# Optimization experiments

Hardware: AMD Instinct MI355X
Metric: run time of the kernel (lower is better)

The kernel has to match this reference:

```python
import jax, jax.numpy as jnp
import numpy as np

EPS = 1e-10

def conv1x1(x, W, b):
    # x:[B,C,H,W], W:[O,C], b:[O]
    return jnp.einsum('bchw,oc->bohw', x, W) + b[None, :, None, None]

def setup_inputs() -> dict:
    key = jax.random.key(0)
    ks = jax.random.split(key, 16)
    B, C, H, W = 8, 512, 32, 32
    R, heads = 4, 8
    s = 1.0 / np.sqrt(C)
    inp = {
        'x': jax.random.normal(ks[0], (B, C, H, W), jnp.float32),
        'u_q': jax.random.uniform(ks[1], (B, R, H, W), jnp.float32, minval=EPS, maxval=1.0),
        'u_k': jax.random.uniform(ks[2], (B, R, H, W), jnp.float32, minval=EPS, maxval=1.0),
        'wq_s': jax.random.normal(ks[3], (R, C), jnp.float32) * s,
        'bq_s': jnp.zeros((R,), jnp.float32),
        'wk_s': jax.random.normal(ks[4], (R, C), jnp.float32) * s,
        'bk_s': jnp.zeros((R,), jnp.float32),
        'Wq': jax.random.normal(ks[5], (C, C), jnp.float32) * s,
        'bq': jnp.zeros((C,), jnp.float32),
        'Wk': jax.random.normal(ks[6], (C, C), jnp.float32) * s,
        'bk': jnp.zeros((C,), jnp.float32),
        'Wv': jax.random.normal(ks[7], (C, C), jnp.float32) * s,
        'bv': jnp.zeros((C,), jnp.float32),
        'Wp': jax.random.normal(ks[8], (C, C), jnp.float32) * s,
        'bp': jnp.zeros((C,), jnp.float32),
    }
    return inp

def reference(x, u_q, u_k, wq_s, bq_s, wk_s, bk_s, Wq, bq, Wk, bk, Wv, bv, Wp, bp):
    B, C, H, W = x.shape
    heads = 8
    hd = C // heads
    scale = hd ** -0.5
    N = H * W

    # gumbel-softmax hard=True then take channel 0 == (argmax(logits+g, dim=1) == 0)
    def sel_mask(ws, bs, u):
        logits = conv1x1(x, ws, bs)                       # [B,R,H,W]
        g = -jnp.log(-jnp.log(u + EPS) + EPS)             # gumbel noise
        m = jnp.argmax(logits + g, axis=1) == 0           # [B,H,W] bool
        return m.reshape(B, N)

    mq = jax.lax.stop_gradient(sel_mask(wq_s, bq_s, u_q))  # selected query points
    mk = jax.lax.stop_gradient(sel_mask(wk_s, bk_s, u_k))  # selected key/value points

    q = conv1x1(x, Wq, bq).reshape(B, heads, hd, N)
    k = conv1x1(x, Wk, bk).reshape(B, heads, hd, N)
    v = conv1x1(x, Wv, bv).reshape(B, heads, hd, N)

    # attention restricted to selected key positions (softmax over masked set
    # == softmax over the gathered subset in the torch code)
    attn = jnp.einsum('bhdn,bhdm->bhnm', q * scale, k)     # [B,h,N,N]
    attn = jnp.where(mk[:, None, None, :], attn, -1e30)
    attn = jax.nn.softmax(attn, axis=-1)
    out = jnp.einsum('bhnm,bhdm->bhdn', attn, v)           # [B,h,hd,N]

    # scatter attention output back into v at the selected query positions
    v_new = jnp.where(mq[:, None, :], out.reshape(B, C, N), v.reshape(B, C, N))
    v_new = v_new.reshape(B, C, H, W)
    return conv1x1(v_new, Wp, bp)
```

## Files before the change

kernel.cpp:

```cpp
#include <hip/hip_runtime.h>
#include <hip/hip_bf16.h>

#define B_ 8
#define C_ 512
#define N_ 1024
#define HEADS_ 8
#define HD_ 64

using f32x4  = __attribute__((ext_vector_type(4))) float;
using bf16x8 = __attribute__((ext_vector_type(8))) __bf16;

__device__ __forceinline__ unsigned short f2bf(float f) {
  union { float f; unsigned u; } v; v.f = f;
  unsigned r = v.u + 0x7FFFu + ((v.u >> 16) & 1u);
  return (unsigned short)(r >> 16);
}

__device__ __forceinline__ void gload16(const void* g, void* l) {
  __builtin_amdgcn_global_load_lds(
      (const __attribute__((address_space(1))) unsigned int*)g,
      (__attribute__((address_space(3))) unsigned int*)l, 16, 0, 0);
}

__global__ __launch_bounds__(256) void k_prep(
    const float* __restrict__ x, const float* __restrict__ u_q, const float* __restrict__ u_k,
    const float* __restrict__ wqs, const float* __restrict__ bqs,
    const float* __restrict__ wks, const float* __restrict__ bks,
    const float* __restrict__ Wq, const float* __restrict__ Wk,
    const float* __restrict__ Wv, const float* __restrict__ Wp,
    unsigned short* __restrict__ xT, unsigned short* __restrict__ wbf,
    unsigned int* __restrict__ sel) {
  __shared__ __align__(16) char smem[25600];
  int id = blockIdx.x;
  int t = threadIdx.x;
  if (id < 256) {
    float* wq_l = (float*)smem;
    float* wk_l = wq_l + 2048;
    float* part = wk_l + 2048;
    int b = id >> 5;
    int n0 = (id & 31) * 32;
    int nl = t & 31, ch = t >> 5;
    for (int i = t; i < 2048; i += 256) {
      wq_l[i] = wqs[i];
      wk_l[i] = wks[i];
    }
    __syncthreads();
    int cbase = ch * 64;
    const float* xp = x + ((size_t)b * C_ + cbase) * N_ + n0 + nl;
    float sq[4] = {0.f, 0.f, 0.f, 0.f};
    float sk[4] = {0.f, 0.f, 0.f, 0.f};
    for (int c = 0; c < 64; c++) {
      float xv = xp[(size_t)c * N_];
#pragma unroll
      for (int r = 0; r < 4; r++) {
        sq[r] = fmaf(wq_l[r * 512 + cbase + c], xv, sq[r]);
        sk[r] = fmaf(wk_l[r * 512 + cbase + c], xv, sk[r]);
      }
    }
    float* pp = part + (ch * 32 + nl) * 9;
#pragma unroll
    for (int r = 0; r < 4; r++) { pp[r] = sq[r]; pp[4 + r] = sk[r]; }
    __syncthreads();
    if (t < 32) {
      int n = n0 + t;
      float fq[4], fk[4];
#pragma unroll
      for (int r = 0; r < 4; r++) { fq[r] = bqs[r]; fk[r] = bks[r]; }
#pragma unroll
      for (int c2 = 0; c2 < 8; c2++) {
        const float* q2 = part + (c2 * 32 + t) * 9;
#pragma unroll
        for (int r = 0; r < 4; r++) { fq[r] += q2[r]; fk[r] += q2[4 + r]; }
      }
#pragma unroll
      for (int r = 0; r < 4; r++) {
        float uq = u_q[((size_t)b * 4 + r) * N_ + n];
        float uk = u_k[((size_t)b * 4 + r) * N_ + n];
        fq[r] += -logf(-logf(uq + 1e-10f) + 1e-10f);
        fk[r] += -logf(-logf(uk + 1e-10f) + 1e-10f);
      }
      bool selq = (fq[0] >= fq[1]) && (fq[0] >= fq[2]) && (fq[0] >= fq[3]);
      bool selk = (fk[0] >= fk[1]) && (fk[0] >= fk[2]) && (fk[0] >= fk[3]);
      sel[(size_t)b * N_ + n] = selq ? 1u : 0u;
      sel[(size_t)(B_ + b) * N_ + n] = selk ? 1u : 0u;
    }
  } else if (id < 1280) {
    float (*tile)[65] = (float(*)[65])smem;
    int m = id - 256;
    int n0 = (m & 15) * 64, c0 = ((m >> 4) & 7) * 64, b = m >> 7;
    int tr = t >> 2, tc = (t & 3) * 16;
    const float* src = x + ((size_t)b * C_ + c0) * N_ + n0;
#pragma unroll
    for (int i = 0; i < 4; i++) {
      float4 v4 = *(const float4*)(src + (size_t)tr * N_ + tc + i * 4);
      tile[tr][tc + i * 4 + 0] = v4.x; tile[tr][tc + i * 4 + 1] = v4.y;
      tile[tr][tc + i * 4 + 2] = v4.z; tile[tr][tc + i * 4 + 3] = v4.w;
    }
    __syncthreads();
    unsigned short* dst = xT + ((size_t)b * N_ + n0) * C_ + c0;
#pragma unroll
    for (int i = 0; i < 4; i++) {
      unsigned short o4[4];
#pragma unroll
      for (int j = 0; j < 4; j++) o4[j] = f2bf(tile[tc + i * 4 + j][tr]);
      unsigned lo = (unsigned)o4[0] | ((unsigned)o4[1] << 16);
      unsigned hi = (unsigned)o4[2] | ((unsigned)o4[3] << 16);
      uint2 u; u.x = lo; u.y = hi;
      *(uint2*)(dst + (size_t)tr * C_ + tc + i * 4) = u;
    }
  } else {
    int i = (id - 1280) * 256 + t;
    int mat = i >> 16, idx4 = i & 65535;
    const float* src = (mat == 0) ? Wq : (mat == 1) ? Wk : (mat == 2) ? Wv : Wp;
    float4 v = ((const float4*)src)[idx4];
    unsigned lo = (unsigned)f2bf(v.x) | ((unsigned)f2bf(v.y) << 16);
    unsigned hi = (unsigned)f2bf(v.z) | ((unsigned)f2bf(v.w) << 16);
    uint2 u; u.x = lo; u.y = hi;
    ((uint2*)wbf)[i] = u;
  }
}

__global__ __launch_bounds__(1024) void k_scan(
    const unsigned int* __restrict__ sel, unsigned int* __restrict__ idx,
    unsigned int* __restrict__ cnt) {
  int which = blockIdx.x, b = blockIdx.y;
  const unsigned int* s = sel + ((size_t)which * B_ + b) * N_;
  unsigned int* ip = idx + ((size_t)which * B_ + b) * N_;
  int t = threadIdx.x, lane = t & 63, w = t >> 6;
  __shared__ unsigned int wtot[16], woff[16], totsh;
  unsigned int f = s[t];
  unsigned long long bal = __ballot(f != 0);
  unsigned int wpre = __popcll(bal & ((1ull << lane) - 1ull));
  if (lane == 0) wtot[w] = (unsigned int)__popcll(bal);
  __syncthreads();
  if (t == 0) {
    unsigned int acc = 0;
#pragma unroll
    for (int i = 0; i < 16; i++) { woff[i] = acc; acc += wtot[i]; }
    totsh = acc;
    cnt[which * B_ + b] = acc;
  }
  __syncthreads();
  unsigned int tot = totsh;
  if (f) ip[woff[w] + wpre] = (unsigned int)t;
  if (t >= (int)tot) ip[t] = 0u;
}

template <int MODE>
__global__ __launch_bounds__(256) void k_gemm(
    const unsigned short* __restrict__ Wall, const unsigned short* __restrict__ Bt,
    const float* __restrict__ bias0, const float* __restrict__ bias1,
    const float* __restrict__ bias2,
    const unsigned int* __restrict__ idx, const unsigned int* __restrict__ cnt,
    void* __restrict__ outv) {
  __shared__ __align__(16) unsigned short a_lds[2][128 * 64];
  __shared__ __align__(16) unsigned short b_lds[2][64 * 64];
  int z = blockIdx.z;
  int mat = (MODE == 0) ? (z >> 3) : 0;
  int b   = (MODE == 0) ? (z & 7) : z;
  int n0 = blockIdx.x * 64;
  if (MODE == 0 && mat < 2 && n0 >= (int)cnt[mat * B_ + b]) return;
  const unsigned short* A = Wall + (size_t)mat * 262144;
  const float* bias = (mat == 0) ? bias0 : (mat == 1) ? bias1 : bias2;
  int m0 = blockIdx.y * 128;
  int t = threadIdx.x, wave = t >> 6, lane = t & 63;
  int wr = (wave >> 1) * 64, wc = (wave & 1) * 32;
  f32x4 acc[4][2] = {};
  int srow = t >> 3, spch = t & 7;
  int lch = spch ^ (srow & 7);
  const unsigned short* aptr[4];
  const unsigned short* bptr[2];
#pragma unroll
  for (int i = 0; i < 4; i++)
    aptr[i] = A + (size_t)(m0 + srow + i * 32) * C_ + lch * 8;
#pragma unroll
  for (int i = 0; i < 2; i++) {
    int grow = n0 + srow + i * 32;
    int srcr = (MODE == 0 && mat < 2) ? (int)idx[((size_t)mat * B_ + b) * N_ + grow] : grow;
    bptr[i] = Bt + ((size_t)b * N_ + srcr) * C_ + lch * 8;
  }
#define STAGE_(buf, kt) do { int k0_ = (kt) * 64;                                          \
    _Pragma("unroll") for (int i_ = 0; i_ < 4; i_++)                                       \
      gload16(aptr[i_] + k0_, (char*)a_lds + (buf) * 16384 + wave * 1024 + i_ * 4096);     \
    _Pragma("unroll") for (int i_ = 0; i_ < 2; i_++)                                       \
      gload16(bptr[i_] + k0_, (char*)b_lds + (buf) * 8192 + wave * 1024 + i_ * 4096);      \
    } while (0)
  STAGE_(0, 0);
  for (int kt = 0; kt < 8; kt++) {
    int cur = kt & 1;
    if (kt < 7) {
      STAGE_(cur ^ 1, kt + 1);
      asm volatile("s_waitcnt vmcnt(6)" ::: "memory");
    } else {
      asm volatile("s_waitcnt vmcnt(0)" ::: "memory");
    }
    __builtin_amdgcn_s_barrier();
    const unsigned short* al = a_lds[cur];
    const unsigned short* bl = b_lds[cur];
#pragma unroll
    for (int ks = 0; ks < 2; ks++) {
      bf16x8 af[4], bfr[2];
#pragma unroll
      for (int mi = 0; mi < 4; mi++) {
        int row = wr + mi * 16 + (lane & 15);
        int pch = (ks * 4 + (lane >> 4)) ^ (row & 7);
        af[mi] = *(const bf16x8*)(al + row * 64 + pch * 8);
      }
#pragma unroll
      for (int ni = 0; ni < 2; ni++) {
        int row = wc + ni * 16 + (lane & 15);
        int pch = (ks * 4 + (lane >> 4)) ^ (row & 7);
        bfr[ni] = *(const bf16x8*)(bl + row * 64 + pch * 8);
      }
#pragma unroll
      for (int mi = 0; mi < 4; mi++)
#pragma unroll
        for (int ni = 0; ni < 2; ni++)
          acc[mi][ni] = __builtin_amdgcn_mfma_f32_16x16x32_bf16(af[mi], bfr[ni], acc[mi][ni], 0, 0, 0);
    }
    __builtin_amdgcn_s_barrier();
  }
#undef STAGE_
  if (MODE == 0) {
    unsigned short* outp = (unsigned short*)outv + (size_t)mat * B_ * N_ * C_ + (size_t)b * N_ * C_;
#pragma unroll
    for (int mi = 0; mi < 4; mi++) {
      int ob = m0 + wr + mi * 16 + ((lane >> 4) << 2);
      float bs[4];
#pragma unroll
      for (int r = 0; r < 4; r++) bs[r] = bias[ob + r];
#pragma unroll
      for (int ni = 0; ni < 2; ni++) {
        int n = n0 + wc + ni * 16 + (lane & 15);
        unsigned short o4[4];
#pragma unroll
        for (int r = 0; r < 4; r++) o4[r] = f2bf(acc[mi][ni][r] + bs[r]);
        unsigned lo = (unsigned)o4[0] | ((unsigned)o4[1] << 16);
        unsigned hi = (unsigned)o4[2] | ((unsigned)o4[3] << 16);
        uint2 u; u.x = lo; u.y = hi;
        *(uint2*)(outp + (size_t)n * C_ + ob) = u;
      }
    }
  } else {
    float* outp = (float*)outv + (size_t)b * C_ * N_;
#pragma unroll
    for (int mi = 0; mi < 4; mi++) {
      int ob = m0 + wr + mi * 16 + ((lane >> 4) << 2);
#pragma unroll
      for (int r = 0; r < 4; r++) {
        float bv = bias[ob + r];
#pragma unroll
        for (int ni = 0; ni < 2; ni++) {
          int n = n0 + wc + ni * 16 + (lane & 15);
          outp[(size_t)(ob + r) * N_ + n] = acc[mi][ni][r] + bv;
        }
      }
    }
  }
}

__global__ __launch_bounds__(256) void k_gather_vt(
    const unsigned short* __restrict__ vT, const unsigned int* __restrict__ idx,
    const unsigned int* __restrict__ cnt, unsigned short* __restrict__ vctr) {
  int b = blockIdx.z;
  unsigned int nk = cnt[B_ + b];
  int j0 = blockIdx.x * 64;
  if (j0 >= (int)nk) return;
  int c0 = blockIdx.y * 64;
  __shared__ unsigned short tile[64][72];
  int t = threadIdx.x, tr = t >> 2, tc = (t & 3) * 16;
  int jj = j0 + tr;
  bool valid = jj < (int)nk;
  unsigned int srow = valid ? idx[((size_t)B_ + b) * N_ + jj] : 0u;
  const unsigned short* src = vT + ((size_t)b * N_ + srow) * C_ + c0;
#pragma unroll
  for (int i = 0; i < 4; i++) {
    ushort4 v4 = {0, 0, 0, 0};
    if (valid) v4 = *(const ushort4*)(src + tc + i * 4);
    tile[tr][tc + i * 4 + 0] = v4.x; tile[tr][tc + i * 4 + 1] = v4.y;
    tile[tr][tc + i * 4 + 2] = v4.z; tile[tr][tc + i * 4 + 3] = v4.w;
  }
  __syncthreads();
  unsigned short* dst = vctr + ((size_t)b * C_ + c0) * N_ + j0;
#pragma unroll
  for (int i = 0; i < 4; i++) {
    unsigned short o4[4];
#pragma unroll
    for (int j = 0; j < 4; j++) o4[j] = tile[tc + i * 4 + j][tr];
    unsigned lo = (unsigned)o4[0] | ((unsigned)o4[1] << 16);
    unsigned hi = (unsigned)o4[2] | ((unsigned)o4[3] << 16);
    uint2 u; u.x = lo; u.y = hi;
    *(uint2*)(dst + (size_t)tr * N_ + tc + i * 4) = u;
  }
}

__global__ __launch_bounds__(256) void k_attn(
    const unsigned short* __restrict__ qc, const unsigned short* __restrict__ kc,
    const unsigned short* __restrict__ vctr, unsigned short* __restrict__ vnew,
    const unsigned int* __restrict__ idx, const unsigned int* __restrict__ cnt) {
  __shared__ __align__(16) unsigned short p_lds[4][16 * 72];
  __shared__ float macc[4][16][65];
  __shared__ float mml[4][2][16];
  int qt = blockIdx.x, h = blockIdx.y, b = blockIdx.z;
  int nq = (int)cnt[b], nk = (int)cnt[B_ + b];
  int q0 = qt * 16;
  if (q0 >= nq) return;
  int t = threadIdx.x, wave = t >> 6, lane = t & 63;
  const unsigned short* qp =
      qc + ((size_t)b * N_ + q0 + (lane & 15)) * C_ + h * HD_ + ((lane >> 4) * 8);
  bf16x8 qf0 = *(const bf16x8*)qp;
  bf16x8 qf1 = *(const bf16x8*)(qp + 32);
  float mrow[4], lrow[4];
  f32x4 acc[4];
#pragma unroll
  for (int r = 0; r < 4; r++) { mrow[r] = -1e30f; lrow[r] = 0.f; }
#pragma unroll
  for (int d = 0; d < 4; d++) acc[d] = f32x4{0.f, 0.f, 0.f, 0.f};
  for (int j0 = wave * 64; j0 < nk; j0 += 256) {
    f32x4 s[4];
#pragma unroll
    for (int nf = 0; nf < 4; nf++) {
      const unsigned short* kp =
          kc + ((size_t)b * N_ + j0 + nf * 16 + (lane & 15)) * C_ + h * HD_ + ((lane >> 4) * 8);
      bf16x8 kf0 = *(const bf16x8*)kp;
      bf16x8 kf1 = *(const bf16x8*)(kp + 32);
      f32x4 z = {0.f, 0.f, 0.f, 0.f};
      z = __builtin_amdgcn_mfma_f32_16x16x32_bf16(qf0, kf0, z, 0, 0, 0);
      z = __builtin_amdgcn_mfma_f32_16x16x32_bf16(qf1, kf1, z, 0, 0, 0);
      float mv = ((j0 + nf * 16 + (lane & 15)) < nk) ? 0.f : -1e30f;
#pragma unroll
      for (int r = 0; r < 4; r++) s[nf][r] = z[r] * 0.125f + mv;
    }
    float alpha[4];
#pragma unroll
    for (int r = 0; r < 4; r++) {
      float mx = fmaxf(fmaxf(s[0][r], s[1][r]), fmaxf(s[2][r], s[3][r]));
      mx = fmaxf(mx, __shfl_xor(mx, 1));
      mx = fmaxf(mx, __shfl_xor(mx, 2));
      mx = fmaxf(mx, __shfl_xor(mx, 4));
      mx = fmaxf(mx, __shfl_xor(mx, 8));
      float mn = fmaxf(mrow[r], mx);
      alpha[r] = __expf(mrow[r] - mn);
      mrow[r] = mn;
      float rs = 0.f;
      int ql = ((lane >> 4) << 2) + r;
#pragma unroll
      for (int nf = 0; nf < 4; nf++) {
        float sv = s[nf][r];
        float p = (sv < -1e29f) ? 0.f : __expf(sv - mn);
        rs += p;
        p_lds[wave][ql * 72 + nf * 16 + (lane & 15)] = f2bf(p);
      }
      rs += __shfl_xor(rs, 1);
      rs += __shfl_xor(rs, 2);
      rs += __shfl_xor(rs, 4);
      rs += __shfl_xor(rs, 8);
      lrow[r] = lrow[r] * alpha[r] + rs;
    }
    bf16x8 pa0 = *(const bf16x8*)&p_lds[wave][(lane & 15) * 72 + ((lane >> 4) * 8)];
    bf16x8 pa1 = *(const bf16x8*)&p_lds[wave][(lane & 15) * 72 + 32 + ((lane >> 4) * 8)];
#pragma unroll
    for (int df = 0; df < 4; df++) {
#pragma unroll
      for (int r = 0; r < 4; r++) acc[df][r] *= alpha[r];
      const unsigned short* vp =
          vctr + ((size_t)b * C_ + h * HD_ + df * 16 + (lane & 15)) * N_ + j0 + ((lane >> 4) * 8);
      bf16x8 vf0 = *(const bf16x8*)vp;
      bf16x8 vf1 = *(const bf16x8*)(vp + 32);
      acc[df] = __builtin_amdgcn_mfma_f32_16x16x32_bf16(pa0, vf0, acc[df], 0, 0, 0);
      acc[df] = __builtin_amdgcn_mfma_f32_16x16x32_bf16(pa1, vf1, acc[df], 0, 0, 0);
    }
  }
#pragma unroll
  for (int df = 0; df < 4; df++)
#pragma unroll
    for (int r = 0; r < 4; r++)
      macc[wave][((lane >> 4) << 2) + r][df * 16 + (lane & 15)] = acc[df][r];
  if ((lane & 15) == 0) {
#pragma unroll
    for (int r = 0; r < 4; r++) {
      mml[wave][0][((lane >> 4) << 2) + r] = mrow[r];
      mml[wave][1][((lane >> 4) << 2) + r] = lrow[r];
    }
  }
  __syncthreads();
  {
    int q = t >> 4, d0 = (t & 15) * 4;
    float mg = fmaxf(fmaxf(mml[0][0][q], mml[1][0][q]), fmaxf(mml[2][0][q], mml[3][0][q]));
    float lg = 0.f, o0 = 0.f, o1 = 0.f, o2 = 0.f, o3 = 0.f;
#pragma unroll
    for (int w = 0; w < 4; w++) {
      float sc = __expf(mml[w][0][q] - mg);
      lg += mml[w][1][q] * sc;
      o0 += macc[w][q][d0 + 0] * sc;
      o1 += macc[w][q][d0 + 1] * sc;
      o2 += macc[w][q][d0 + 2] * sc;
      o3 += macc[w][q][d0 + 3] * sc;
    }
    if (q0 + q < nq) {
      unsigned int qrow = idx[(size_t)b * N_ + q0 + q];
      float inv = 1.0f / lg;
      unsigned short o4[4] = {f2bf(o0 * inv), f2bf(o1 * inv), f2bf(o2 * inv), f2bf(o3 * inv)};
      unsigned lo = (unsigned)o4[0] | ((unsigned)o4[1] << 16);
      unsigned hi = (unsigned)o4[2] | ((unsigned)o4[3] << 16);
      uint2 u; u.x = lo; u.y = hi;
      *(uint2*)(vnew + ((size_t)b * N_ + qrow) * C_ + h * HD_ + d0) = u;
    }
  }
}

extern "C" void kernel_launch(void* const* d_in, const int* in_sizes, int n_in,
                              void* d_out, int out_size, void* d_ws, size_t ws_size,
                              hipStream_t stream) {
  const float* x   = (const float*)d_in[0];
  const float* u_q = (const float*)d_in[1];
  const float* u_k = (const float*)d_in[2];
  const float* wqs = (const float*)d_in[3];
  const float* bqs = (const float*)d_in[4];
  const float* wks = (const float*)d_in[5];
  const float* bks = (const float*)d_in[6];
  const float* Wq  = (const float*)d_in[7];
  const float* bq  = (const float*)d_in[8];
  const float* Wk  = (const float*)d_in[9];
  const float* bk  = (const float*)d_in[10];
  const float* Wv  = (const float*)d_in[11];
  const float* bv  = (const float*)d_in[12];
  const float* Wp  = (const float*)d_in[13];
  const float* bp  = (const float*)d_in[14];

  char* ws = (char*)d_ws;
  unsigned short* xT   = (unsigned short*)(ws);
  unsigned short* wbf  = (unsigned short*)(ws + 8388608);
  unsigned short* qkv  = (unsigned short*)(ws + 10485760);
  unsigned short* qc   = qkv;
  unsigned short* kc   = qkv + (size_t)B_ * N_ * C_;
  unsigned short* vT   = kc + (size_t)B_ * N_ * C_;
  unsigned short* vctr = (unsigned short*)(ws + 35651584);
  unsigned int*   sel  = (unsigned int*)(ws + 44040192);
  unsigned int*   idx  = (unsigned int*)(ws + 44105728);
  unsigned int*   cnt  = (unsigned int*)(ws + 44171264);

  k_prep<<<dim3(2304), 256, 0, stream>>>(x, u_q, u_k, wqs, bqs, wks, bks,
                                         Wq, Wk, Wv, Wp, xT, wbf, sel);
  k_scan<<<dim3(2, 8), 1024, 0, stream>>>(sel, idx, cnt);
  k_gemm<0><<<dim3(16, 4, 24), 256, 0, stream>>>(wbf, xT, bq, bk, bv, idx, cnt, (void*)qkv);
  k_gather_vt<<<dim3(16, 8, 8), 256, 0, stream>>>(vT, idx, cnt, vctr);
  k_attn<<<dim3(64, 8, 8), 256, 0, stream>>>(qc, kc, vctr, vT, idx, cnt);
  k_gemm<1><<<dim3(16, 4, 8), 256, 0, stream>>>(wbf + 3 * 262144, vT, bp, bp, bp, idx, cnt, d_out);
}
```

Baseline: 164.5 us.

## Fuse V gather-transpose into QKV GEMM epilogue and shrink GEMM M-tile

```diff
diff --git a/kernel.cpp b/kernel.cpp
--- a/kernel.cpp
+++ b/kernel.cpp
@@ -122,10 +122,11 @@
 
 __global__ __launch_bounds__(1024) void k_scan(
     const unsigned int* __restrict__ sel, unsigned int* __restrict__ idx,
-    unsigned int* __restrict__ cnt) {
+    unsigned int* __restrict__ rnk, unsigned int* __restrict__ cnt) {
   int which = blockIdx.x, b = blockIdx.y;
   const unsigned int* s = sel + ((size_t)which * B_ + b) * N_;
   unsigned int* ip = idx + ((size_t)which * B_ + b) * N_;
+  unsigned int* rp = rnk + ((size_t)which * B_ + b) * N_;
   int t = threadIdx.x, lane = t & 63, w = t >> 6;
   __shared__ unsigned int wtot[16], woff[16], totsh;
   unsigned int f = s[t];
@@ -142,7 +143,11 @@
   }
   __syncthreads();
   unsigned int tot = totsh;
-  if (f) ip[woff[w] + wpre] = (unsigned int)t;
+  if (f) {
+    unsigned int r = woff[w] + wpre;
+    ip[r] = (unsigned int)t;
+    rp[t] = r;
+  }
   if (t >= (int)tot) ip[t] = 0u;
 }
 
@@ -152,8 +157,10 @@
     const float* __restrict__ bias0, const float* __restrict__ bias1,
     const float* __restrict__ bias2,
     const unsigned int* __restrict__ idx, const unsigned int* __restrict__ cnt,
+    const unsigned int* __restrict__ sel, const unsigned int* __restrict__ rnk,
+    unsigned short* __restrict__ vctr,
     void* __restrict__ outv) {
-  __shared__ __align__(16) unsigned short a_lds[2][128 * 64];
+  __shared__ __align__(16) unsigned short a_lds[2][64 * 64];
   __shared__ __align__(16) unsigned short b_lds[2][64 * 64];
   int z = blockIdx.z;
   int mat = (MODE == 0) ? (z >> 3) : 0;
@@ -162,35 +169,32 @@
   if (MODE == 0 && mat < 2 && n0 >= (int)cnt[mat * B_ + b]) return;
   const unsigned short* A = Wall + (size_t)mat * 262144;
   const float* bias = (mat == 0) ? bias0 : (mat == 1) ? bias1 : bias2;
-  int m0 = blockIdx.y * 128;
+  int m0 = blockIdx.y * 64;
   int t = threadIdx.x, wave = t >> 6, lane = t & 63;
-  int wr = (wave >> 1) * 64, wc = (wave & 1) * 32;
-  f32x4 acc[4][2] = {};
+  int wr = (wave >> 1) * 32, wc = (wave & 1) * 32;
+  f32x4 acc[2][2] = {};
   int srow = t >> 3, spch = t & 7;
   int lch = spch ^ (srow & 7);
-  const unsigned short* aptr[4];
+  const unsigned short* aptr[2];
   const unsigned short* bptr[2];
 #pragma unroll
-  for (int i = 0; i < 4; i++)
+  for (int i = 0; i < 2; i++) {
     aptr[i] = A + (size_t)(m0 + srow + i * 32) * C_ + lch * 8;
-#pragma unroll
-  for (int i = 0; i < 2; i++) {
     int grow = n0 + srow + i * 32;
     int srcr = (MODE == 0 && mat < 2) ? (int)idx[((size_t)mat * B_ + b) * N_ + grow] : grow;
     bptr[i] = Bt + ((size_t)b * N_ + srcr) * C_ + lch * 8;
   }
 #define STAGE_(buf, kt) do { int k0_ = (kt) * 64;                                          \
-    _Pragma("unroll") for (int i_ = 0; i_ < 4; i_++)                                       \
-      gload16(aptr[i_] + k0_, (char*)a_lds + (buf) * 16384 + wave * 1024 + i_ * 4096);     \
-    _Pragma("unroll") for (int i_ = 0; i_ < 2; i_++)                                       \
+    _Pragma("unroll") for (int i_ = 0; i_ < 2; i_++) {                                     \
+      gload16(aptr[i_] + k0_, (char*)a_lds + (buf) * 8192 + wave * 1024 + i_ * 4096);      \
       gload16(bptr[i_] + k0_, (char*)b_lds + (buf) * 8192 + wave * 1024 + i_ * 4096);      \
-    } while (0)
+    } } while (0)
   STAGE_(0, 0);
   for (int kt = 0; kt < 8; kt++) {
     int cur = kt & 1;
     if (kt < 7) {
       STAGE_(cur ^ 1, kt + 1);
-      asm volatile("s_waitcnt vmcnt(6)" ::: "memory");
+      asm volatile("s_waitcnt vmcnt(4)" ::: "memory");
     } else {
       asm volatile("s_waitcnt vmcnt(0)" ::: "memory");
     }
@@ -199,9 +203,9 @@
     const unsigned short* bl = b_lds[cur];
 #pragma unroll
     for (int ks = 0; ks < 2; ks++) {
-      bf16x8 af[4], bfr[2];
-#pragma unroll
-      for (int mi = 0; mi < 4; mi++) {
+      bf16x8 af[2], bfr[2];
+#pragma unroll
+      for (int mi = 0; mi < 2; mi++) {
         int row = wr + mi * 16 + (lane & 15);
         int pch = (ks * 4 + (lane >> 4)) ^ (row & 7);
         af[mi] = *(const bf16x8*)(al + row * 64 + pch * 8);
@@ -213,7 +217,7 @@
         bfr[ni] = *(const bf16x8*)(bl + row * 64 + pch * 8);
       }
 #pragma unroll
-      for (int mi = 0; mi < 4; mi++)
+      for (int mi = 0; mi < 2; mi++)
 #pragma unroll
         for (int ni = 0; ni < 2; ni++)
           acc[mi][ni] = __builtin_amdgcn_mfma_f32_16x16x32_bf16(af[mi], bfr[ni], acc[mi][ni], 0, 0, 0);
@@ -224,7 +228,7 @@
   if (MODE == 0) {
     unsigned short* outp = (unsigned short*)outv + (size_t)mat * B_ * N_ * C_ + (size_t)b * N_ * C_;
 #pragma unroll
-    for (int mi = 0; mi < 4; mi++) {
+    for (int mi = 0; mi < 2; mi++) {
       int ob = m0 + wr + mi * 16 + ((lane >> 4) << 2);
       float bs[4];
 #pragma unroll
@@ -239,12 +243,20 @@
         unsigned hi = (unsigned)o4[2] | ((unsigned)o4[3] << 16);
         uint2 u; u.x = lo; u.y = hi;
         *(uint2*)(outp + (size_t)n * C_ + ob) = u;
+        if (mat == 2) {
+          if (sel[(size_t)(B_ + b) * N_ + n]) {
+            unsigned int j = rnk[(size_t)(B_ + b) * N_ + n];
+#pragma unroll
+            for (int r = 0; r < 4; r++)
+              vctr[((size_t)b * C_ + ob + r) * N_ + j] = o4[r];
+          }
+        }
       }
     }
   } else {
     float* outp = (float*)outv + (size_t)b * C_ * N_;
 #pragma unroll
-    for (int mi = 0; mi < 4; mi++) {
+    for (int mi = 0; mi < 2; mi++) {
       int ob = m0 + wr + mi * 16 + ((lane >> 4) << 2);
 #pragma unroll
       for (int r = 0; r < 4; r++) {
@@ -256,41 +268,6 @@
         }
       }
     }
-  }
-}
-
-__global__ __launch_bounds__(256) void k_gather_vt(
-    const unsigned short* __restrict__ vT, const unsigned int* __restrict__ idx,
-    const unsigned int* __restrict__ cnt, unsigned short* __restrict__ vctr) {
-  int b = blockIdx.z;
-  unsigned int nk = cnt[B_ + b];
-  int j0 = blockIdx.x * 64;
-  if (j0 >= (int)nk) return;
-  int c0 = blockIdx.y * 64;
-  __shared__ unsigned short tile[64][72];
-  int t = threadIdx.x, tr = t >> 2, tc = (t & 3) * 16;
-  int jj = j0 + tr;
-  bool valid = jj < (int)nk;
-  unsigned int srow = valid ? idx[((size_t)B_ + b) * N_ + jj] : 0u;
-  const unsigned short* src = vT + ((size_t)b * N_ + srow) * C_ + c0;
-#pragma unroll
-  for (int i = 0; i < 4; i++) {
-    ushort4 v4 = {0, 0, 0, 0};
-    if (valid) v4 = *(const ushort4*)(src + tc + i * 4);
-    tile[tr][tc + i * 4 + 0] = v4.x; tile[tr][tc + i * 4 + 1] = v4.y;
-    tile[tr][tc + i * 4 + 2] = v4.z; tile[tr][tc + i * 4 + 3] = v4.w;
-  }
-  __syncthreads();
-  unsigned short* dst = vctr + ((size_t)b * C_ + c0) * N_ + j0;
-#pragma unroll
-  for (int i = 0; i < 4; i++) {
-    unsigned short o4[4];
-#pragma unroll
-    for (int j = 0; j < 4; j++) o4[j] = tile[tc + i * 4 + j][tr];
-    unsigned lo = (unsigned)o4[0] | ((unsigned)o4[1] << 16);
-    unsigned hi = (unsigned)o4[2] | ((unsigned)o4[3] << 16);
-    uint2 u; u.x = lo; u.y = hi;
-    *(uint2*)(dst + (size_t)tr * N_ + tc + i * 4) = u;
   }
 }
 
@@ -438,13 +415,15 @@
   unsigned short* vctr = (unsigned short*)(ws + 35651584);
   unsigned int*   sel  = (unsigned int*)(ws + 44040192);
   unsigned int*   idx  = (unsigned int*)(ws + 44105728);
-  unsigned int*   cnt  = (unsigned int*)(ws + 44171264);
+  unsigned int*   rnk  = (unsigned int*)(ws + 44171264);
+  unsigned int*   cnt  = (unsigned int*)(ws + 44236800);
 
   k_prep<<<dim3(2304), 256, 0, stream>>>(x, u_q, u_k, wqs, bqs, wks, bks,
                                          Wq, Wk, Wv, Wp, xT, wbf, sel);
-  k_scan<<<dim3(2, 8), 1024, 0, stream>>>(sel, idx, cnt);
-  k_gemm<0><<<dim3(16, 4, 24), 256, 0, stream>>>(wbf, xT, bq, bk, bv, idx, cnt, (void*)qkv);
-  k_gather_vt<<<dim3(16, 8, 8), 256, 0, stream>>>(vT, idx, cnt, vctr);
+  k_scan<<<dim3(2, 8), 1024, 0, stream>>>(sel, idx, rnk, cnt);
+  k_gemm<0><<<dim3(16, 8, 24), 256, 0, stream>>>(wbf, xT, bq, bk, bv, idx, cnt,
+                                                 sel, rnk, vctr, (void*)qkv);
   k_attn<<<dim3(64, 8, 8), 256, 0, stream>>>(qc, kc, vctr, vT, idx, cnt);
-  k_gemm<1><<<dim3(16, 4, 8), 256, 0, stream>>>(wbf + 3 * 262144, vT, bp, bp, bp, idx, cnt, d_out);
-}
+  k_gemm<1><<<dim3(16, 8, 8), 256, 0, stream>>>(wbf + 3 * 262144, vT, bp, bp, bp, idx, cnt,
+                                                sel, rnk, vctr, d_out);
+}
```

Result: no change. 165.6 us (+0.6%).
